# Performance work log

Hardware: AMD Instinct MI355X
Metric: run time of the kernel (lower is better)

## Reference

```python
import jax, jax.numpy as jnp
import numpy as np

N = 50000   # num_nodes
E = 250000  # edges per view
D = 128     # in_dim = h_dim = out_dim
B = 4       # num_bases
RELS = (8, 12, 6)


def setup_inputs() -> dict:
    key = jax.random.key(0)
    ks = iter(jax.random.split(key, 64))
    s = 1.0 / np.sqrt(D)
    inp = {"node_features": jax.random.normal(next(ks), (N, D), jnp.float32) * 0.1}
    for v, R in enumerate(RELS, start=1):
        inp[f"src{v}"] = jax.random.randint(next(ks), (E,), 0, N)
        inp[f"dst{v}"] = jax.random.randint(next(ks), (E,), 0, N)
        inp[f"rel{v}"] = jax.random.randint(next(ks), (E,), 0, R)
        for l in (1, 2):
            inp[f"v{v}_bases{l}"] = jax.random.normal(next(ks), (B, D, D), jnp.float32) * s
            inp[f"v{v}_coef{l}"] = jax.random.normal(next(ks), (R, B), jnp.float32) * 0.5
            inp[f"v{v}_loopw{l}"] = jax.random.normal(next(ks), (D, D), jnp.float32) * s
            inp[f"v{v}_bias{l}"] = jnp.zeros((D,), jnp.float32)
    inp["fusion_w"] = jax.random.normal(next(ks), (3 * D, D), jnp.float32) * (1.0 / np.sqrt(3 * D))
    inp["fusion_b"] = jnp.zeros((D,), jnp.float32)
    return inp


def rgcn_layer(h, src, dst, rel, bases, coef, loop_w, bias, act):
    # basis trick: project nodes through all bases once, then combine per edge
    node_proj = jnp.einsum('ni,bio->nbo', h, bases)          # [N,B,out]
    msg = jnp.einsum('eb,ebo->eo', coef[rel], node_proj[src])  # [E,out]
    agg = jax.ops.segment_sum(msg, dst, num_segments=h.shape[0])
    out = agg + h @ loop_w + bias                             # self-loop + bias (DGL defaults)
    return jax.nn.relu(out) if act else out


def single_view(feats, src, dst, rel, bases1, coef1, loopw1, bias1,
                bases2, coef2, loopw2, bias2):
    h = rgcn_layer(feats, src, dst, rel, bases1, coef1, loopw1, bias1, act=True)
    return rgcn_layer(h, src, dst, rel, bases2, coef2, loopw2, bias2, act=False)


def reference(node_features,
              src1, dst1, rel1, src2, dst2, rel2, src3, dst3, rel3,
              v1_bases1, v1_coef1, v1_loopw1, v1_bias1,
              v1_bases2, v1_coef2, v1_loopw2, v1_bias2,
              v2_bases1, v2_coef1, v2_loopw1, v2_bias1,
              v2_bases2, v2_coef2, v2_loopw2, v2_bias2,
              v3_bases1, v3_coef1, v3_loopw1, v3_bias1,
              v3_bases2, v3_coef2, v3_loopw2, v3_bias2,
              fusion_w, fusion_b):
    h1 = single_view(node_features, src1, dst1, rel1,
                     v1_bases1, v1_coef1, v1_loopw1, v1_bias1,
                     v1_bases2, v1_coef2, v1_loopw2, v1_bias2)
    h2 = single_view(node_features, src2, dst2, rel2,
                     v2_bases1, v2_coef1, v2_loopw1, v2_bias1,
                     v2_bases2, v2_coef2, v2_loopw2, v2_bias2)
    h3 = single_view(node_features, src3, dst3, rel3,
                     v3_bases1, v3_coef1, v3_loopw1, v3_bias1,
                     v3_bases2, v3_coef2, v3_loopw2, v3_bias2)
    h_cat = jnp.concatenate([h1, h2, h3], axis=-1)  # [N, 3*D]
    return h_cat @ fusion_w + fusion_b
```

## Files before the change

### kernel.cpp

```cpp
#include <hip/hip_runtime.h>
#include <hip/hip_bf16.h>
#include <stdint.h>

typedef _Float16 f16x8 __attribute__((ext_vector_type(8)));
typedef _Float16 f16x2 __attribute__((ext_vector_type(2)));
typedef float f32x4 __attribute__((ext_vector_type(4)));


__device__ __forceinline__ void gll16(const _Float16* g, _Float16* l) {
    __builtin_amdgcn_global_load_lds(
        (const __attribute__((address_space(1))) void*)g,
        (__attribute__((address_space(3))) void*)l, 16, 0, 0);
}

struct PrepDesc { const float* src; _Float16* dst; int dstride; };
struct PrepArgs { PrepDesc d[33]; };

__global__ __launch_bounds__(256) void prep_weights(PrepArgs args) {
    __shared__ _Float16 lds[128 * 129];
    const PrepDesc de = args.d[blockIdx.x];
    int t = threadIdx.x;
    for (int q = 0; q < 64; ++q) {
        int li = t + q * 256;
        int i = li >> 7, o = li & 127;
        lds[o * 129 + i] = (_Float16)de.src[li];
    }
    __syncthreads();
    for (int q = 0; q < 64; ++q) {
        int lo = t + q * 256;
        int o = lo >> 7, i = lo & 127;
        de.dst[(size_t)o * de.dstride + (i ^ ((o & 7) << 3))] = lds[o * 129 + i];
    }
}

__global__ __launch_bounds__(256) void f32_to_f16(const float* __restrict__ in,
                                                  _Float16* __restrict__ out, int n4) {
    int i = blockIdx.x * 256 + threadIdx.x;
    if (i >= n4) return;
    float4 v = *((const float4*)in + i);
    int n = i >> 5;
    int c = (i & 31) * 4;
    int cs = c ^ ((n & 7) << 3);
    f16x2 a, b;
    a[0] = (_Float16)v.x; a[1] = (_Float16)v.y;
    b[0] = (_Float16)v.z; b[1] = (_Float16)v.w;
    _Float16* o = out + (size_t)n * 128 + cs;
    *(f16x2*)o = a;
    *(f16x2*)(o + 2) = b;
}

struct EdgeArgs {
    const int* src[3]; const int* dst[3]; const int* rel[3];
    int E[3]; int N;
};

__global__ __launch_bounds__(256) void bhist(EdgeArgs ea, int* __restrict__ hmat, int nbk) {
    __shared__ int cnt[256];
    int v = blockIdx.y, blk = blockIdx.x, t = threadIdx.x;
    cnt[t] = 0;
    __syncthreads();
    int E = ea.E[v];
    const int* dst = ea.dst[v];
    int chunk = (E + 63) >> 6;
    int e0 = blk * chunk;
    int e1 = min(e0 + chunk, E);
    for (int e = e0 + t; e < e1; e += 256)
        atomicAdd(&cnt[dst[e] >> 8], 1);
    __syncthreads();
    if (t < nbk)
        hmat[((size_t)v * nbk + t) * 64 + blk] = cnt[t];
}

__global__ __launch_bounds__(256) void scan1_kernel(const int* __restrict__ deg,
                                                    int* __restrict__ off,
                                                    int* __restrict__ bsum, int n) {
    __shared__ int s[256];
    int b = blockIdx.x, t = threadIdx.x;
    int base = b * 2048 + t * 8;
    int v[8]; int sum = 0;
    for (int j = 0; j < 8; ++j) {
        int x = (base + j < n) ? deg[base + j] : 0;
        v[j] = sum;
        sum += x;
    }
    s[t] = sum;
    __syncthreads();
    for (int st = 1; st < 256; st <<= 1) {
        int y = (t >= st) ? s[t - st] : 0;
        __syncthreads();
        s[t] += y;
        __syncthreads();
    }
    int texcl = t ? s[t - 1] : 0;
    if (t == 255) bsum[b] = s[255];
    for (int j = 0; j < 8; ++j)
        if (base + j < n) off[base + j] = texcl + v[j];
}

__global__ __launch_bounds__(256) void scan2b(int* __restrict__ off,
                                              const int* __restrict__ bsum,
                                              int n, int Etot) {
    __shared__ int pref;
    int b = blockIdx.x, t = threadIdx.x;
    if (t == 0) { int p = 0; for (int j = 0; j < b; ++j) p += bsum[j]; pref = p; }
    __syncthreads();
    int p = pref;
    int base = b * 2048 + t * 8;
    for (int j = 0; j < 8; ++j)
        if (base + j < n) off[base + j] += p;
    if (b == 0 && t == 0) off[n] = Etot;
}

__global__ __launch_bounds__(256) void bscat(EdgeArgs ea, const int* __restrict__ smat,
                                             int* __restrict__ mid, int nbk) {
    __shared__ int cur[256];
    int v = blockIdx.y, blk = blockIdx.x, t = threadIdx.x;
    if (t < nbk) cur[t] = smat[((size_t)v * nbk + t) * 64 + blk];
    __syncthreads();
    int E = ea.E[v];
    const int* src = ea.src[v];
    const int* dst = ea.dst[v];
    const int* rel = ea.rel[v];
    int chunk = (E + 63) >> 6;
    int e0 = blk * chunk;
    int e1 = min(e0 + chunk, E);
    for (int e = e0 + t; e < e1; e += 256) {
        int d = dst[e];
        int pos = atomicAdd(&cur[d >> 8], 1);
        mid[pos] = src[e] | (rel[e] << 16) | ((d & 255) << 20);
    }
}

__global__ __launch_bounds__(256) void bfinal(const int* __restrict__ smat,
                                              const int* __restrict__ mid,
                                              int* __restrict__ off3,
                                              int* __restrict__ packed3,
                                              int M, int nbk, int Etot) {
    __shared__ int cnt[256];
    __shared__ int s[256];
    __shared__ int cur[256];
    int bk = blockIdx.x, v = blockIdx.y, t = threadIdx.x;
    int flat0 = (v * nbk + bk) * 64;
    int start = smat[flat0];
    int end   = smat[flat0 + 64];
    cnt[t] = 0;
    __syncthreads();
    for (int i = start + t; i < end; i += 256)
        atomicAdd(&cnt[(mid[i] >> 20) & 255], 1);
    __syncthreads();
    s[t] = cnt[t];
    __syncthreads();
    for (int st = 1; st < 256; st <<= 1) {
        int y = (t >= st) ? s[t - st] : 0;
        __syncthreads();
        s[t] += y;
        __syncthreads();
    }
    int excl = t ? s[t - 1] : 0;
    int node = (bk << 8) + t;
    if (node < M) off3[(size_t)v * M + node] = start + excl;
    cur[t] = start + excl;
    __syncthreads();
    for (int i = start + t; i < end; i += 256) {
        int m = mid[i];
        int pos = atomicAdd(&cur[(m >> 20) & 255], 1);
        packed3[pos] = (m & 0xFFFF) | (((m >> 16) & 15) << 20);
    }
    if (v == 2 && bk == nbk - 1 && t == 0) off3[(size_t)3 * M] = Etot;
}

struct GatherArgs {
    const int* off3;
    const int* packed3;
    const float* coef[3];
    const _Float16* h[3];
    _Float16* T;
    int N; size_t Tvs;
};

__global__ __launch_bounds__(256) void gather3(GatherArgs g) {
    int v = blockIdx.y;
    int wid = threadIdx.x >> 6;
    int lane = threadIdx.x & 63;
    int nodeA = blockIdx.x * 8 + wid * 2;
    if (nodeA >= g.N) return;
    int nodeB = nodeA + 1;
    bool hasB = nodeB < g.N;

    const int* off = g.off3 + (size_t)v * g.N;
    const float* coef = g.coef[v];
    const _Float16* h = g.h[v];
    _Float16* T = g.T + (size_t)v * g.Tvs;

    int iA = __builtin_amdgcn_readfirstlane(off[nodeA]);
    int eA = __builtin_amdgcn_readfirstlane(off[nodeA + 1]);
    int iB = eA;
    int eB = hasB ? __builtin_amdgcn_readfirstlane(off[nodeB + 1]) : eA;

    float accA[8] = {}, accB[8] = {};

    auto edge1 = [&](int p, float* acc) {
        int s = p & 0xFFFFF, r = p >> 20;
        uint32_t q = ((const uint32_t*)(h + (size_t)s * 128))[lane ^ ((s & 7) << 2)];
        float4 c = *(const float4*)(coef + (size_t)r * 4);
        f16x2 u = __builtin_bit_cast(f16x2, q);
        float lo = (float)u[0], hi = (float)u[1];
        acc[0] += c.x * lo;  acc[1] += c.x * hi;
        acc[2] += c.y * lo;  acc[3] += c.y * hi;
        acc[4] += c.z * lo;  acc[5] += c.z * hi;
        acc[6] += c.w * lo;  acc[7] += c.w * hi;
    };

    for (; iA + 1 < eA && iB + 1 < eB; iA += 2, iB += 2) {
        int pA0 = __builtin_amdgcn_readfirstlane(g.packed3[iA]);
        int pA1 = __builtin_amdgcn_readfirstlane(g.packed3[iA + 1]);
        int pB0 = __builtin_amdgcn_readfirstlane(g.packed3[iB]);
        int pB1 = __builtin_amdgcn_readfirstlane(g.packed3[iB + 1]);
        int sA0 = pA0 & 0xFFFFF, sA1 = pA1 & 0xFFFFF;
        int sB0 = pB0 & 0xFFFFF, sB1 = pB1 & 0xFFFFF;
        uint32_t qA0 = ((const uint32_t*)(h + (size_t)sA0 * 128))[lane ^ ((sA0 & 7) << 2)];
        uint32_t qA1 = ((const uint32_t*)(h + (size_t)sA1 * 128))[lane ^ ((sA1 & 7) << 2)];
        uint32_t qB0 = ((const uint32_t*)(h + (size_t)sB0 * 128))[lane ^ ((sB0 & 7) << 2)];
        uint32_t qB1 = ((const uint32_t*)(h + (size_t)sB1 * 128))[lane ^ ((sB1 & 7) << 2)];
        float4 cA0 = *(const float4*)(coef + (size_t)(pA0 >> 20) * 4);
        float4 cA1 = *(const float4*)(coef + (size_t)(pA1 >> 20) * 4);
        float4 cB0 = *(const float4*)(coef + (size_t)(pB0 >> 20) * 4);
        float4 cB1 = *(const float4*)(coef + (size_t)(pB1 >> 20) * 4);
        f16x2 u;
        float lo, hi;
        u = __builtin_bit_cast(f16x2, qA0); lo = (float)u[0]; hi = (float)u[1];
        accA[0] += cA0.x * lo; accA[1] += cA0.x * hi; accA[2] += cA0.y * lo; accA[3] += cA0.y * hi;
        accA[4] += cA0.z * lo; accA[5] += cA0.z * hi; accA[6] += cA0.w * lo; accA[7] += cA0.w * hi;
        u = __builtin_bit_cast(f16x2, qA1); lo = (float)u[0]; hi = (float)u[1];
        accA[0] += cA1.x * lo; accA[1] += cA1.x * hi; accA[2] += cA1.y * lo; accA[3] += cA1.y * hi;
        accA[4] += cA1.z * lo; accA[5] += cA1.z * hi; accA[6] += cA1.w * lo; accA[7] += cA1.w * hi;
        u = __builtin_bit_cast(f16x2, qB0); lo = (float)u[0]; hi = (float)u[1];
        accB[0] += cB0.x * lo; accB[1] += cB0.x * hi; accB[2] += cB0.y * lo; accB[3] += cB0.y * hi;
        accB[4] += cB0.z * lo; accB[5] += cB0.z * hi; accB[6] += cB0.w * lo; accB[7] += cB0.w * hi;
        u = __builtin_bit_cast(f16x2, qB1); lo = (float)u[0]; hi = (float)u[1];
        accB[0] += cB1.x * lo; accB[1] += cB1.x * hi; accB[2] += cB1.y * lo; accB[3] += cB1.y * hi;
        accB[4] += cB1.z * lo; accB[5] += cB1.z * hi; accB[6] += cB1.w * lo; accB[7] += cB1.w * hi;
    }
    for (; iA + 1 < eA; iA += 2) {
        int p0 = __builtin_amdgcn_readfirstlane(g.packed3[iA]);
        int p1 = __builtin_amdgcn_readfirstlane(g.packed3[iA + 1]);
        edge1(p0, accA); edge1(p1, accA);
    }
    for (; iA < eA; ++iA)
        edge1(__builtin_amdgcn_readfirstlane(g.packed3[iA]), accA);
    for (; iB + 1 < eB; iB += 2) {
        int p0 = __builtin_amdgcn_readfirstlane(g.packed3[iB]);
        int p1 = __builtin_amdgcn_readfirstlane(g.packed3[iB + 1]);
        edge1(p0, accB); edge1(p1, accB);
    }
    for (; iB < eB; ++iB)
        edge1(__builtin_amdgcn_readfirstlane(g.packed3[iB]), accB);

    {
        int cs = (2 * lane) ^ ((nodeA & 7) << 3);
        _Float16* tb = T + (size_t)nodeA * 512 + cs;
        for (int b = 0; b < 4; ++b) {
            f16x2 o; o[0] = (_Float16)accA[2 * b]; o[1] = (_Float16)accA[2 * b + 1];
            *(f16x2*)(tb + b * 128) = o;
        }
    }
    if (hasB) {
        int cs = (2 * lane) ^ ((nodeB & 7) << 3);
        _Float16* tb = T + (size_t)nodeB * 512 + cs;
        for (int b = 0; b < 4; ++b) {
            f16x2 o; o[0] = (_Float16)accB[2 * b]; o[1] = (_Float16)accB[2 * b + 1];
            *(f16x2*)(tb + b * 128) = o;
        }
    }
}

struct GemmArgs {
    const _Float16* T;
    const _Float16* hin[3];
    const _Float16* WT[3];
    const float* bias[3];
    _Float16* hout;
    int M; int relu; size_t Tvs; size_t hovs;
};

__global__ __launch_bounds__(512) void gemm_layer(GemmArgs ga) {
    __shared__ _Float16 As[64 * 128];
    __shared__ _Float16 Bs[128 * 128];
    int v = blockIdx.y;
    const _Float16* Tb  = ga.T + (size_t)v * ga.Tvs;
    const _Float16* hin = ga.hin[v];
    const _Float16* BT  = ga.WT[v];
    const float* bias   = ga.bias[v];
    _Float16* out       = ga.hout + (size_t)v * ga.hovs;
    int M = ga.M;

    int tid = threadIdx.x;
    int m0 = blockIdx.x * 64;
    int wid = tid >> 6, lane = tid & 63;
    int wr = (wid >> 2) * 32;
    int wc = (wid & 3) * 32;
    int lm = lane & 15;
    int lk = (lane >> 4) * 8;
    int xm = (lm & 7) << 3;

    f32x4 acc[2][2] = {};

    for (int kb = 0; kb < 5; ++kb) {
        const _Float16* Asrc; size_t astride;
        if (kb < 4) { Asrc = Tb + (size_t)kb * 128; astride = 512; }
        else        { Asrc = hin;                   astride = 128; }
        for (int q = 0; q < 2; ++q) {
            int li = tid + q * 512;
            int r = li >> 4;
            int c = (li & 15) << 3;
            int gr = m0 + r; if (gr >= M) gr = M - 1;
            gll16(Asrc + (size_t)gr * astride + c, As + (size_t)li * 8);
        }
        for (int q = 0; q < 4; ++q) {
            int li = tid + q * 512;
            gll16(BT + (size_t)(li >> 4) * 640 + kb * 128 + ((li & 15) << 3),
                  Bs + (size_t)li * 8);
        }
        __syncthreads();

        for (int ks = 0; ks < 4; ++ks) {
            int ac = (ks * 32 + lk) ^ xm;
            f16x8 a[2], b[2];
            for (int mi = 0; mi < 2; ++mi)
                a[mi] = *(const f16x8*)(As + (wr + mi * 16 + lm) * 128 + ac);
            for (int ni = 0; ni < 2; ++ni)
                b[ni] = *(const f16x8*)(Bs + (wc + ni * 16 + lm) * 128 + ac);
            for (int mi = 0; mi < 2; ++mi)
                for (int ni = 0; ni < 2; ++ni)
                    acc[mi][ni] = __builtin_amdgcn_mfma_f32_16x16x32_f16(a[mi], b[ni], acc[mi][ni], 0, 0, 0);
        }
        __syncthreads();
    }

    int rbase = (lane >> 4) * 4;
    for (int mi = 0; mi < 2; ++mi) {
        for (int j = 0; j < 4; ++j) {
            int gr = m0 + wr + mi * 16 + rbase + j;
            if (gr >= M) continue;
            int rs = (gr & 7) << 3;
            for (int ni = 0; ni < 2; ++ni) {
                int col = wc + ni * 16 + lm;
                float val = acc[mi][ni][j] + bias[col];
                if (ga.relu) val = fmaxf(val, 0.f);
                out[(size_t)gr * 128 + (col ^ rs)] = (_Float16)val;
            }
        }
    }
}

struct FusArgs {
    const _Float16* A[3];
    const _Float16* BT;
    const float* bias;
    float* out; int M;
};

__global__ __launch_bounds__(256) void gemm_fusion(FusArgs fa) {
    __shared__ _Float16 As[128 * 128];
    __shared__ _Float16 Bs[128 * 128];
    int tid = threadIdx.x;
    int m0 = blockIdx.x * 128;
    int M = fa.M;
    int wid = tid >> 6, lane = tid & 63;
    int wr = (wid >> 1) * 64;
    int wc = (wid & 1) * 64;
    int lm = lane & 15;
    int lk = (lane >> 4) * 8;
    int xm = (lm & 7) << 3;

    f32x4 acc[4][4] = {};

    for (int kb = 0; kb < 3; ++kb) {
        const _Float16* Asrc = fa.A[kb];
        for (int q = 0; q < 8; ++q) {
            int li = tid + q * 256;
            int r = li >> 4;
            int c = (li & 15) << 3;
            int gr = m0 + r; if (gr >= M) gr = M - 1;
            gll16(Asrc + (size_t)gr * 128 + c, As + (size_t)li * 8);
        }
        for (int q = 0; q < 8; ++q) {
            int li = tid + q * 256;
            gll16(fa.BT + (size_t)(li >> 4) * 384 + kb * 128 + ((li & 15) << 3),
                  Bs + (size_t)li * 8);
        }
        __syncthreads();

        for (int ks = 0; ks < 4; ++ks) {
            int ac = (ks * 32 + lk) ^ xm;
            f16x8 a[4], b[4];
            for (int mi = 0; mi < 4; ++mi)
                a[mi] = *(const f16x8*)(As + (wr + mi * 16 + lm) * 128 + ac);
            for (int ni = 0; ni < 4; ++ni)
                b[ni] = *(const f16x8*)(Bs + (wc + ni * 16 + lm) * 128 + ac);
            for (int mi = 0; mi < 4; ++mi)
                for (int ni = 0; ni < 4; ++ni)
                    acc[mi][ni] = __builtin_amdgcn_mfma_f32_16x16x32_f16(a[mi], b[ni], acc[mi][ni], 0, 0, 0);
        }
        __syncthreads();
    }

    int rbase = (lane >> 4) * 4;
    for (int mi = 0; mi < 4; ++mi) {
        for (int j = 0; j < 4; ++j) {
            int gr = m0 + wr + mi * 16 + rbase + j;
            if (gr >= M) continue;
            for (int ni = 0; ni < 4; ++ni) {
                int col = wc + ni * 16 + lm;
                fa.out[(size_t)gr * 128 + col] = acc[mi][ni][j] + fa.bias[col];
            }
        }
    }
}

extern "C" void kernel_launch(void* const* d_in, const int* in_sizes, int n_in,
                              void* d_out, int out_size, void* d_ws, size_t ws_size,
                              hipStream_t stream) {
    const int D = 128;
    const int M = in_sizes[0] / D;

    struct ViewIn {
        const int *src, *dst, *rel;
        const float *bases1, *coef1, *loopw1, *bias1;
        const float *bases2, *coef2, *loopw2, *bias2;
        int E;
    } V[3];
    int idx = 1;
    for (int v = 0; v < 3; ++v) {
        V[v].src    = (const int*)d_in[idx + 0];
        V[v].dst    = (const int*)d_in[idx + 1];
        V[v].rel    = (const int*)d_in[idx + 2];
        V[v].bases1 = (const float*)d_in[idx + 3];
        V[v].coef1  = (const float*)d_in[idx + 4];
        V[v].loopw1 = (const float*)d_in[idx + 5];
        V[v].bias1  = (const float*)d_in[idx + 6];
        V[v].bases2 = (const float*)d_in[idx + 7];
        V[v].coef2  = (const float*)d_in[idx + 8];
        V[v].loopw2 = (const float*)d_in[idx + 9];
        V[v].bias2  = (const float*)d_in[idx + 10];
        V[v].E      = in_sizes[idx + 0];
        idx += 11;
    }
    const float* fusion_w = (const float*)d_in[idx];
    const float* fusion_b = (const float*)d_in[idx + 1];
    int Etot = V[0].E + V[1].E + V[2].E;

    int nbk = (M + 255) >> 8;
    int nsc = 3 * nbk * 64;

    char* w = (char*)d_ws;
    auto alloc = [&](size_t bytes) -> char* {
        char* p = w; w += (bytes + 255) & ~(size_t)255; return p;
    };
    _Float16* nf16 = (_Float16*)alloc((size_t)M * 128 * 2);
    _Float16* wts  = (_Float16*)alloc((size_t)(6 * 81920 + 49152) * 2);
    int* hmat      = (int*)alloc((size_t)nsc * 4);
    int* smat      = (int*)alloc(((size_t)nsc + 1) * 4);
    int* bsum      = (int*)alloc(512);
    int* off3      = (int*)alloc(((size_t)3 * M + 1) * 4);
    int* mid       = (int*)alloc((size_t)Etot * 4);
    int* packed3   = (int*)alloc((size_t)Etot * 4);
    _Float16* T3   = (_Float16*)alloc((size_t)3 * M * 512 * 2);
    _Float16* h1b  = (_Float16*)alloc((size_t)3 * M * 128 * 2);
    _Float16* h2b  = (_Float16*)alloc((size_t)3 * M * 128 * 2);

    _Float16 *WT[3][2];
    for (int v = 0; v < 3; ++v)
        for (int l = 0; l < 2; ++l)
            WT[v][l] = wts + (size_t)(v * 2 + l) * 81920;
    _Float16* fusTcat = wts + 6 * 81920;

    PrepArgs pa;
    int t = 0;
    for (int v = 0; v < 3; ++v) {
        const float* bases[2] = { V[v].bases1, V[v].bases2 };
        const float* loopw[2] = { V[v].loopw1, V[v].loopw2 };
        for (int l = 0; l < 2; ++l) {
            for (int b = 0; b < 4; ++b) {
                pa.d[t].src = bases[l] + (size_t)b * 16384;
                pa.d[t].dst = WT[v][l] + (size_t)b * 128;
                pa.d[t].dstride = 640; ++t;
            }
            pa.d[t].src = loopw[l];
            pa.d[t].dst = WT[v][l] + 512;
            pa.d[t].dstride = 640; ++t;
        }
    }
    for (int v = 0; v < 3; ++v) {
        pa.d[t].src = fusion_w + (size_t)v * 16384;
        pa.d[t].dst = fusTcat + (size_t)v * 128;
        pa.d[t].dstride = 384; ++t;
    }
    prep_weights<<<33, 256, 0, stream>>>(pa);

    int n4 = M * D / 4;
    f32_to_f16<<<(n4 + 255) / 256, 256, 0, stream>>>((const float*)d_in[0], nf16, n4);

    EdgeArgs ea;
    for (int v = 0; v < 3; ++v) {
        ea.src[v] = V[v].src; ea.dst[v] = V[v].dst; ea.rel[v] = V[v].rel; ea.E[v] = V[v].E;
    }
    ea.N = M;
    int nsb = (nsc + 2047) / 2048;
    bhist<<<dim3(64, 3), 256, 0, stream>>>(ea, hmat, nbk);
    scan1_kernel<<<nsb, 256, 0, stream>>>(hmat, smat, bsum, nsc);
    scan2b<<<nsb, 256, 0, stream>>>(smat, bsum, nsc, Etot);
    bscat<<<dim3(64, 3), 256, 0, stream>>>(ea, smat, mid, nbk);
    bfinal<<<dim3(nbk, 3), 256, 0, stream>>>(smat, mid, off3, packed3, M, nbk, Etot);

    int ng  = (M + 7) / 8;
    int gxL = (M + 63) / 64;
    int gxF = (M + 127) / 128;
    size_t Tvs = (size_t)M * 512;
    size_t hvs = (size_t)M * 128;
    float* outF = (float*)d_out;

    GatherArgs g1;
    g1.off3 = off3; g1.packed3 = packed3; g1.T = T3; g1.N = M; g1.Tvs = Tvs;
    for (int v = 0; v < 3; ++v) { g1.coef[v] = V[v].coef1; g1.h[v] = nf16; }
    gather3<<<dim3(ng, 3), 256, 0, stream>>>(g1);

    GemmArgs m1;
    m1.T = T3; m1.hout = h1b; m1.M = M; m1.relu = 1; m1.Tvs = Tvs; m1.hovs = hvs;
    for (int v = 0; v < 3; ++v) { m1.hin[v] = nf16; m1.WT[v] = WT[v][0]; m1.bias[v] = V[v].bias1; }
    gemm_layer<<<dim3(gxL, 3), 512, 0, stream>>>(m1);

    GatherArgs g2 = g1;
    for (int v = 0; v < 3; ++v) { g2.coef[v] = V[v].coef2; g2.h[v] = h1b + (size_t)v * hvs; }
    gather3<<<dim3(ng, 3), 256, 0, stream>>>(g2);

    GemmArgs m2;
    m2.T = T3; m2.hout = h2b; m2.M = M; m2.relu = 0; m2.Tvs = Tvs; m2.hovs = hvs;
    for (int v = 0; v < 3; ++v) { m2.hin[v] = h1b + (size_t)v * hvs; m2.WT[v] = WT[v][1]; m2.bias[v] = V[v].bias2; }
    gemm_layer<<<dim3(gxL, 3), 512, 0, stream>>>(m2);

    FusArgs fa;
    for (int v = 0; v < 3; ++v) fa.A[v] = h2b + (size_t)v * hvs;
    fa.BT = fusTcat; fa.bias = fusion_b; fa.out = outF; fa.M = M;
    gemm_fusion<<<gxF, 256, 0, stream>>>(fa);
}
```

Measured before the change: 288.8 us.

## Fold layer-2 weights into fusion weights and fuse layer-2 GEMM with fusion GEMM

New measurement: 300.2 us. 4.0% more time.

```diff
diff --git a/kernel.cpp b/kernel.cpp
--- a/kernel.cpp
+++ b/kernel.cpp
@@ -31,6 +31,76 @@
         int o = lo >> 7, i = lo & 127;
         de.dst[(size_t)o * de.dstride + (i ^ ((o & 7) << 3))] = lds[o * 129 + i];
     }
+}
+
+struct FoldArgs {
+    const float* bases2[3];
+    const float* loopw2[3];
+    const float* fw;
+    _Float16* W2F[3];
+};
+
+__global__ __launch_bounds__(256) void fold_w2f(FoldArgs fa) {
+    __shared__ _Float16 As[128 * 136];
+    __shared__ _Float16 Bs[128 * 136];
+    int c = blockIdx.x, v = blockIdx.y, t = threadIdx.x;
+    const float* A = (c < 4) ? fa.bases2[v] + (size_t)c * 16384 : fa.loopw2[v];
+    for (int q = 0; q < 64; ++q) {
+        int li = t + q * 256;
+        int i = li >> 7, o2 = li & 127;
+        As[i * 136 + o2] = (_Float16)A[li];
+    }
+    for (int q = 0; q < 64; ++q) {
+        int li = t + q * 256;
+        int o2 = li >> 7, of = li & 127;
+        Bs[of * 136 + o2] = (_Float16)fa.fw[(size_t)(v * 128 + o2) * 128 + of];
+    }
+    __syncthreads();
+
+    int wid = t >> 6, lane = t & 63;
+    int wr = (wid >> 1) * 64;
+    int wc = (wid & 1) * 64;
+    int lm = lane & 15;
+    int lk = (lane >> 4) * 8;
+
+    f32x4 acc[4][4] = {};
+    for (int ks = 0; ks < 4; ++ks) {
+        f16x8 a[4], b[4];
+        for (int mi = 0; mi < 4; ++mi)
+            a[mi] = *(const f16x8*)(As + (wr + mi * 16 + lm) * 136 + ks * 32 + lk);
+        for (int ni = 0; ni < 4; ++ni)
+            b[ni] = *(const f16x8*)(Bs + (wc + ni * 16 + lm) * 136 + ks * 32 + lk);
+        for (int mi = 0; mi < 4; ++mi)
+            for (int ni = 0; ni < 4; ++ni)
+                acc[mi][ni] = __builtin_amdgcn_mfma_f32_16x16x32_f16(a[mi], b[ni], acc[mi][ni], 0, 0, 0);
+    }
+
+    int rbase = (lane >> 4) * 4;
+    _Float16* dst = fa.W2F[v];
+    for (int mi = 0; mi < 4; ++mi) {
+        for (int j = 0; j < 4; ++j) {
+            int i = wr + mi * 16 + rbase + j;
+            for (int ni = 0; ni < 4; ++ni) {
+                int of = wc + ni * 16 + lm;
+                dst[(size_t)of * 640 + c * 128 + (i ^ ((of & 7) << 3))] = (_Float16)acc[mi][ni][j];
+            }
+        }
+    }
+}
+
+__global__ __launch_bounds__(128) void fold_bias(const float* __restrict__ fb,
+                                                 const float* __restrict__ fw,
+                                                 const float* __restrict__ b2_0,
+                                                 const float* __restrict__ b2_1,
+                                                 const float* __restrict__ b2_2,
+                                                 float* __restrict__ bias_out) {
+    int of = threadIdx.x;
+    const float* b2[3] = { b2_0, b2_1, b2_2 };
+    float s = fb[of];
+    for (int v = 0; v < 3; ++v)
+        for (int o2 = 0; o2 < 128; ++o2)
+            s += b2[v][o2] * fw[(size_t)(v * 128 + o2) * 128 + of];
+    bias_out[of] = s;
 }
 
 __global__ __launch_bounds__(256) void f32_to_f16(const float* __restrict__ in,
@@ -353,66 +423,74 @@
     }
 }
 
-struct FusArgs {
-    const _Float16* A[3];
-    const _Float16* BT;
+struct L2FArgs {
+    const _Float16* T;
+    const _Float16* h1;
+    const _Float16* W2F[3];
     const float* bias;
-    float* out; int M;
+    float* out; int M; size_t Tvs; size_t hvs;
 };
 
-__global__ __launch_bounds__(256) void gemm_fusion(FusArgs fa) {
-    __shared__ _Float16 As[128 * 128];
+__global__ __launch_bounds__(512) void gemm_l2f(L2FArgs ga) {
+    __shared__ _Float16 As[64 * 128];
     __shared__ _Float16 Bs[128 * 128];
+    int M = ga.M;
     int tid = threadIdx.x;
-    int m0 = blockIdx.x * 128;
-    int M = fa.M;
+    int m0 = blockIdx.x * 64;
     int wid = tid >> 6, lane = tid & 63;
-    int wr = (wid >> 1) * 64;
-    int wc = (wid & 1) * 64;
+    int wr = (wid >> 2) * 32;
+    int wc = (wid & 3) * 32;
     int lm = lane & 15;
     int lk = (lane >> 4) * 8;
     int xm = (lm & 7) << 3;
 
-    f32x4 acc[4][4] = {};
-
-    for (int kb = 0; kb < 3; ++kb) {
-        const _Float16* Asrc = fa.A[kb];
-        for (int q = 0; q < 8; ++q) {
-            int li = tid + q * 256;
-            int r = li >> 4;
-            int c = (li & 15) << 3;
-            int gr = m0 + r; if (gr >= M) gr = M - 1;
-            gll16(Asrc + (size_t)gr * 128 + c, As + (size_t)li * 8);
-        }
-        for (int q = 0; q < 8; ++q) {
-            int li = tid + q * 256;
-            gll16(fa.BT + (size_t)(li >> 4) * 384 + kb * 128 + ((li & 15) << 3),
-                  Bs + (size_t)li * 8);
-        }
-        __syncthreads();
-
-        for (int ks = 0; ks < 4; ++ks) {
-            int ac = (ks * 32 + lk) ^ xm;
-            f16x8 a[4], b[4];
-            for (int mi = 0; mi < 4; ++mi)
-                a[mi] = *(const f16x8*)(As + (wr + mi * 16 + lm) * 128 + ac);
-            for (int ni = 0; ni < 4; ++ni)
-                b[ni] = *(const f16x8*)(Bs + (wc + ni * 16 + lm) * 128 + ac);
-            for (int mi = 0; mi < 4; ++mi)
-                for (int ni = 0; ni < 4; ++ni)
-                    acc[mi][ni] = __builtin_amdgcn_mfma_f32_16x16x32_f16(a[mi], b[ni], acc[mi][ni], 0, 0, 0);
-        }
-        __syncthreads();
+    f32x4 acc[2][2] = {};
+
+    for (int v = 0; v < 3; ++v) {
+        const _Float16* Tb = ga.T + (size_t)v * ga.Tvs;
+        const _Float16* hb = ga.h1 + (size_t)v * ga.hvs;
+        const _Float16* BT = ga.W2F[v];
+        for (int kb = 0; kb < 5; ++kb) {
+            const _Float16* Asrc; size_t astride;
+            if (kb < 4) { Asrc = Tb + (size_t)kb * 128; astride = 512; }
+            else        { Asrc = hb;                    astride = 128; }
+            for (int q = 0; q < 2; ++q) {
+                int li = tid + q * 512;
+                int r = li >> 4;
+                int c = (li & 15) << 3;
+                int gr = m0 + r; if (gr >= M) gr = M - 1;
+                gll16(Asrc + (size_t)gr * astride + c, As + (size_t)li * 8);
+            }
+            for (int q = 0; q < 4; ++q) {
+                int li = tid + q * 512;
+                gll16(BT + (size_t)(li >> 4) * 640 + kb * 128 + ((li & 15) << 3),
+                      Bs + (size_t)li * 8);
+            }
+            __syncthreads();
+
+            for (int ks = 0; ks < 4; ++ks) {
+                int ac = (ks * 32 + lk) ^ xm;
+                f16x8 a[2], b[2];
+                for (int mi = 0; mi < 2; ++mi)
+                    a[mi] = *(const f16x8*)(As + (wr + mi * 16 + lm) * 128 + ac);
+                for (int ni = 0; ni < 2; ++ni)
+                    b[ni] = *(const f16x8*)(Bs + (wc + ni * 16 + lm) * 128 + ac);
+                for (int mi = 0; mi < 2; ++mi)
+                    for (int ni = 0; ni < 2; ++ni)
+                        acc[mi][ni] = __builtin_amdgcn_mfma_f32_16x16x32_f16(a[mi], b[ni], acc[mi][ni], 0, 0, 0);
+            }
+            __syncthreads();
+        }
     }
 
     int rbase = (lane >> 4) * 4;
-    for (int mi = 0; mi < 4; ++mi) {
+    for (int mi = 0; mi < 2; ++mi) {
         for (int j = 0; j < 4; ++j) {
             int gr = m0 + wr + mi * 16 + rbase + j;
             if (gr >= M) continue;
-            for (int ni = 0; ni < 4; ++ni) {
+            for (int ni = 0; ni < 2; ++ni) {
                 int col = wc + ni * 16 + lm;
-                fa.out[(size_t)gr * 128 + col] = acc[mi][ni][j] + fa.bias[col];
+                ga.out[(size_t)gr * 128 + col] = acc[mi][ni][j] + ga.bias[col];
             }
         }
     }
@@ -458,7 +536,9 @@
         char* p = w; w += (bytes + 255) & ~(size_t)255; return p;
     };
     _Float16* nf16 = (_Float16*)alloc((size_t)M * 128 * 2);
-    _Float16* wts  = (_Float16*)alloc((size_t)(6 * 81920 + 49152) * 2);
+    _Float16* wts  = (_Float16*)alloc((size_t)(3 * 81920) * 2);
+    _Float16* w2f  = (_Float16*)alloc((size_t)(3 * 81920) * 2);
+    float* bias_o  = (float*)alloc(128 * 4);
     int* hmat      = (int*)alloc((size_t)nsc * 4);
     int* smat      = (int*)alloc(((size_t)nsc + 1) * 4);
     int* bsum      = (int*)alloc(512);
@@ -467,36 +547,37 @@
     int* packed3   = (int*)alloc((size_t)Etot * 4);
     _Float16* T3   = (_Float16*)alloc((size_t)3 * M * 512 * 2);
     _Float16* h1b  = (_Float16*)alloc((size_t)3 * M * 128 * 2);
-    _Float16* h2b  = (_Float16*)alloc((size_t)3 * M * 128 * 2);
-
-    _Float16 *WT[3][2];
-    for (int v = 0; v < 3; ++v)
-        for (int l = 0; l < 2; ++l)
-            WT[v][l] = wts + (size_t)(v * 2 + l) * 81920;
-    _Float16* fusTcat = wts + 6 * 81920;
+
+    _Float16 *WT1[3], *W2F[3];
+    for (int v = 0; v < 3; ++v) {
+        WT1[v] = wts + (size_t)v * 81920;
+        W2F[v] = w2f + (size_t)v * 81920;
+    }
 
     PrepArgs pa;
     int t = 0;
     for (int v = 0; v < 3; ++v) {
-        const float* bases[2] = { V[v].bases1, V[v].bases2 };
-        const float* loopw[2] = { V[v].loopw1, V[v].loopw2 };
-        for (int l = 0; l < 2; ++l) {
-            for (int b = 0; b < 4; ++b) {
-                pa.d[t].src = bases[l] + (size_t)b * 16384;
-                pa.d[t].dst = WT[v][l] + (size_t)b * 128;
-                pa.d[t].dstride = 640; ++t;
-            }
-            pa.d[t].src = loopw[l];
-            pa.d[t].dst = WT[v][l] + 512;
+        for (int b = 0; b < 4; ++b) {
+            pa.d[t].src = V[v].bases1 + (size_t)b * 16384;
+            pa.d[t].dst = WT1[v] + (size_t)b * 128;
             pa.d[t].dstride = 640; ++t;
         }
-    }
+        pa.d[t].src = V[v].loopw1;
+        pa.d[t].dst = WT1[v] + 512;
+        pa.d[t].dstride = 640; ++t;
+    }
+    prep_weights<<<t, 256, 0, stream>>>(pa);
+
+    FoldArgs fo;
     for (int v = 0; v < 3; ++v) {
-        pa.d[t].src = fusion_w + (size_t)v * 16384;
-        pa.d[t].dst = fusTcat + (size_t)v * 128;
-        pa.d[t].dstride = 384; ++t;
-    }
-    prep_weights<<<33, 256, 0, stream>>>(pa);
+        fo.bases2[v] = V[v].bases2;
+        fo.loopw2[v] = V[v].loopw2;
+        fo.W2F[v] = W2F[v];
+    }
+    fo.fw = fusion_w;
+    fold_w2f<<<dim3(5, 3), 256, 0, stream>>>(fo);
+    fold_bias<<<1, 128, 0, stream>>>(fusion_b, fusion_w,
+                                     V[0].bias2, V[1].bias2, V[2].bias2, bias_o);
 
     int n4 = M * D / 4;
     f32_to_f16<<<(n4 + 255) / 256, 256, 0, stream>>>((const float*)d_in[0], nf16, n4);
@@ -515,7 +596,6 @@
 
     int ng  = (M + 7) / 8;
     int gxL = (M + 63) / 64;
-    int gxF = (M + 127) / 128;
     size_t Tvs = (size_t)M * 512;
     size_t hvs = (size_t)M * 128;
     float* outF = (float*)d_out;
@@ -527,20 +607,16 @@
 
     GemmArgs m1;
     m1.T = T3; m1.hout = h1b; m1.M = M; m1.relu = 1; m1.Tvs = Tvs; m1.hovs = hvs;
-    for (int v = 0; v < 3; ++v) { m1.hin[v] = nf16; m1.WT[v] = WT[v][0]; m1.bias[v] = V[v].bias1; }
+    for (int v = 0; v < 3; ++v) { m1.hin[v] = nf16; m1.WT[v] = WT1[v]; m1.bias[v] = V[v].bias1; }
     gemm_layer<<<dim3(gxL, 3), 512, 0, stream>>>(m1);
 
     GatherArgs g2 = g1;
     for (int v = 0; v < 3; ++v) { g2.coef[v] = V[v].coef2; g2.h[v] = h1b + (size_t)v * hvs; }
     gather3<<<dim3(ng, 3), 256, 0, stream>>>(g2);
 
-    GemmArgs m2;
-    m2.T = T3; m2.hout = h2b; m2.M = M; m2.relu = 0; m2.Tvs = Tvs; m2.hovs = hvs;
-    for (int v = 0; v < 3; ++v) { m2.hin[v] = h1b + (size_t)v * hvs; m2.WT[v] = WT[v][1]; m2.bias[v] = V[v].bias2; }
-    gemm_layer<<<dim3(gxL, 3), 512, 0, stream>>>(m2);
-
-    FusArgs fa;
-    for (int v = 0; v < 3; ++v) fa.A[v] = h2b + (size_t)v * hvs;
-    fa.BT = fusTcat; fa.bias = fusion_b; fa.out = outF; fa.M = M;
-    gemm_fusion<<<gxF, 256, 0, stream>>>(fa);
-}
+    L2FArgs l2;
+    l2.T = T3; l2.h1 = h1b; l2.bias = bias_o; l2.out = outF;
+    l2.M = M; l2.Tvs = Tvs; l2.hvs = hvs;
+    for (int v = 0; v < 3; ++v) l2.W2F[v] = W2F[v];
+    gemm_l2f<<<gxL, 512, 0, stream>>>(l2);
+}
```
